# Kernel optimization log

Measured on AMD Instinct MI355X. Metric: run time of the kernel, lower is better.

## Reference

```python
import jax, jax.numpy as jnp
import numpy as np

B, C, K = 256, 4096, 32

def setup_inputs() -> dict:
    key = jax.random.key(0)
    k1, k2, k3 = jax.random.split(key, 3)
    input_data = jax.random.normal(k1, (B, C), dtype=jnp.float32)
    adaptive_margin = jax.random.uniform(k2, (B, C), dtype=jnp.float32)
    # labels in [-1, C); -1 entries are padding (masked out, as in the torch code)
    target = jax.random.randint(k3, (B, K), -1, C, dtype=jnp.int64)
    return {"input_data": input_data, "adaptive_margin": adaptive_margin, "target": target}

def reference(input_data, adaptive_margin, target):
    # input_data, adaptive_margin: [B, C]; target: [B, K] with -1 padding
    Bc, Cc = input_data.shape
    valid = target > -1                                  # [B, K]
    t_idx = jnp.where(valid, target, 0)                  # safe gather index
    m_t = jnp.take_along_axis(adaptive_margin, t_idx, axis=1)  # [B, K]
    x_t = jnp.take_along_axis(input_data, t_idx, axis=1)       # [B, K]
    # pairwise: 1 + (m_t - m_j) - (x_t - x_j) over all classes j, [B, K, C]
    diff = 1.0 + (m_t[:, :, None] - adaptive_margin[:, None, :]) \
               - (x_t[:, :, None] - input_data[:, None, :])
    # exclude j == t and padded labels
    cls = jnp.arange(Cc, dtype=target.dtype)
    keep = valid[:, :, None] & (cls[None, None, :] != t_idx[:, :, None])
    loss = jnp.sum(jnp.where(keep, jax.nn.relu(diff), 0.0))
    return loss / Cc  # size_average=False (default)
```

## Files before the change

### kernel.cpp

```cpp
#include <hip/hip_runtime.h>


#define BB 256
#define CC 4096
#define KK 32
#define THREADS 256

__global__ __launch_bounds__(THREADS) void mlam_rows(
    const float* __restrict__ input,
    const float* __restrict__ margin,
    const int* __restrict__ target,
    float* __restrict__ partials) {

    __shared__ float sc[CC];
    __shared__ float sa[KK];
    __shared__ int   svalid;
    __shared__ float swave[THREADS / 64];

    const int b   = blockIdx.x;
    const int tid = threadIdx.x;
    const float* in_row = input  + (size_t)b * CC;
    const float* mg_row = margin + (size_t)b * CC;

    const float4* in4 = (const float4*)in_row;
    const float4* mg4 = (const float4*)mg_row;
    float4* sc4 = (float4*)sc;
#pragma unroll
    for (int i = 0; i < CC / 4 / THREADS; ++i) {
        int idx = tid + i * THREADS;
        float4 x = in4[idx];
        float4 m = mg4[idx];
        sc4[idx] = make_float4(x.x - m.x, x.y - m.y, x.z - m.z, x.w - m.w);
    }
    if (tid == 0) svalid = 0;
    __syncthreads();

    if (tid < KK) {
        int t = target[b * KK + tid];
        if (t >= 0) {
            sa[tid] = 1.0f + mg_row[t] - in_row[t];
            atomicAdd(&svalid, 1);
        } else {
            sa[tid] = -1e30f;
        }
    }
    __syncthreads();

    float a[KK];
#pragma unroll
    for (int k = 0; k < KK; ++k) a[k] = sa[k];

    float acc = 0.0f;
#pragma unroll
    for (int i = 0; i < CC / 4 / THREADS; ++i) {
        float4 c = sc4[tid + i * THREADS];
#pragma unroll
        for (int k = 0; k < KK; ++k) {
            acc += fmaxf(a[k] + c.x, 0.0f);
            acc += fmaxf(a[k] + c.y, 0.0f);
            acc += fmaxf(a[k] + c.z, 0.0f);
            acc += fmaxf(a[k] + c.w, 0.0f);
        }
    }

#pragma unroll
    for (int off = 32; off > 0; off >>= 1)
        acc += __shfl_down(acc, off, 64);
    if ((tid & 63) == 0) swave[tid >> 6] = acc;
    __syncthreads();
    if (tid == 0) {
        float tot = 0.0f;
#pragma unroll
        for (int w = 0; w < THREADS / 64; ++w) tot += swave[w];
        partials[b] = tot - (float)svalid;
    }
}

__global__ __launch_bounds__(THREADS) void mlam_reduce(
    const float* __restrict__ partials,
    float* __restrict__ out) {
    __shared__ float swave[THREADS / 64];
    const int tid = threadIdx.x;
    float v = partials[tid];
#pragma unroll
    for (int off = 32; off > 0; off >>= 1)
        v += __shfl_down(v, off, 64);
    if ((tid & 63) == 0) swave[tid >> 6] = v;
    __syncthreads();
    if (tid == 0) {
        float tot = 0.0f;
#pragma unroll
        for (int w = 0; w < THREADS / 64; ++w) tot += swave[w];
        out[0] = tot * (1.0f / (float)CC);
    }
}

extern "C" void kernel_launch(void* const* d_in, const int* in_sizes, int n_in,
                              void* d_out, int out_size, void* d_ws, size_t ws_size,
                              hipStream_t stream) {
    const float* input  = (const float*)d_in[0];
    const float* margin = (const float*)d_in[1];
    const int*   target = (const int*)d_in[2];
    float* out      = (float*)d_out;
    float* partials = (float*)d_ws;

    mlam_rows<<<BB, THREADS, 0, stream>>>(input, margin, target, partials);
    mlam_reduce<<<1, THREADS, 0, stream>>>(partials, out);
}
```

Measured before the change: 66.23 us.

## Fuse row and reduce kernels with atomic accumulation and one column per thread

Raises block size to 1024 threads so each thread holds exactly one float4 of the row in registers, which removes the shared-memory staging buffer. The separate reduction kernel is dropped: each block atomically adds its scaled partial into the output, which is zeroed by a memset first. Four independent accumulators break the serial add dependency chain. The memset adds a stream operation, and float atomics make the summation order nondeterministic.

After: 66.47 us. Within noise of the previous version (+0.4%).

```diff
diff --git a/kernel.cpp b/kernel.cpp
--- a/kernel.cpp
+++ b/kernel.cpp
@@ -4,34 +4,28 @@
 #define BB 256
 #define CC 4096
 #define KK 32
-#define THREADS 256
+#define THREADS 1024
+#define NWAVES (THREADS / 64)
 
-__global__ __launch_bounds__(THREADS) void mlam_rows(
+__global__ __launch_bounds__(THREADS) void mlam_fused(
     const float* __restrict__ input,
     const float* __restrict__ margin,
     const int* __restrict__ target,
-    float* __restrict__ partials) {
+    float* __restrict__ out) {
 
-    __shared__ float sc[CC];
     __shared__ float sa[KK];
     __shared__ int   svalid;
-    __shared__ float swave[THREADS / 64];
+    __shared__ float swave[NWAVES];
 
     const int b   = blockIdx.x;
     const int tid = threadIdx.x;
     const float* in_row = input  + (size_t)b * CC;
     const float* mg_row = margin + (size_t)b * CC;
 
-    const float4* in4 = (const float4*)in_row;
-    const float4* mg4 = (const float4*)mg_row;
-    float4* sc4 = (float4*)sc;
-#pragma unroll
-    for (int i = 0; i < CC / 4 / THREADS; ++i) {
-        int idx = tid + i * THREADS;
-        float4 x = in4[idx];
-        float4 m = mg4[idx];
-        sc4[idx] = make_float4(x.x - m.x, x.y - m.y, x.z - m.z, x.w - m.w);
-    }
+    float4 x = ((const float4*)in_row)[tid];
+    float4 m = ((const float4*)mg_row)[tid];
+    float4 c = make_float4(x.x - m.x, x.y - m.y, x.z - m.z, x.w - m.w);
+
     if (tid == 0) svalid = 0;
     __syncthreads();
 
@@ -50,18 +44,16 @@
 #pragma unroll
     for (int k = 0; k < KK; ++k) a[k] = sa[k];
 
-    float acc = 0.0f;
+    float acc0 = 0.f, acc1 = 0.f, acc2 = 0.f, acc3 = 0.f;
 #pragma unroll
-    for (int i = 0; i < CC / 4 / THREADS; ++i) {
-        float4 c = sc4[tid + i * THREADS];
-#pragma unroll
-        for (int k = 0; k < KK; ++k) {
-            acc += fmaxf(a[k] + c.x, 0.0f);
-            acc += fmaxf(a[k] + c.y, 0.0f);
-            acc += fmaxf(a[k] + c.z, 0.0f);
-            acc += fmaxf(a[k] + c.w, 0.0f);
-        }
+    for (int k = 0; k < KK; ++k) {
+        float ak = a[k];
+        acc0 += fmaxf(ak + c.x, 0.0f);
+        acc1 += fmaxf(ak + c.y, 0.0f);
+        acc2 += fmaxf(ak + c.z, 0.0f);
+        acc3 += fmaxf(ak + c.w, 0.0f);
     }
+    float acc = (acc0 + acc1) + (acc2 + acc3);
 
 #pragma unroll
     for (int off = 32; off > 0; off >>= 1)
@@ -71,27 +63,8 @@
     if (tid == 0) {
         float tot = 0.0f;
 #pragma unroll
-        for (int w = 0; w < THREADS / 64; ++w) tot += swave[w];
-        partials[b] = tot - (float)svalid;
-    }
-}
-
-__global__ __launch_bounds__(THREADS) void mlam_reduce(
-    const float* __restrict__ partials,
-    float* __restrict__ out) {
-    __shared__ float swave[THREADS / 64];
-    const int tid = threadIdx.x;
-    float v = partials[tid];
-#pragma unroll
-    for (int off = 32; off > 0; off >>= 1)
-        v += __shfl_down(v, off, 64);
-    if ((tid & 63) == 0) swave[tid >> 6] = v;
-    __syncthreads();
-    if (tid == 0) {
-        float tot = 0.0f;
-#pragma unroll
-        for (int w = 0; w < THREADS / 64; ++w) tot += swave[w];
-        out[0] = tot * (1.0f / (float)CC);
+        for (int w = 0; w < NWAVES; ++w) tot += swave[w];
+        atomicAdd(out, (tot - (float)svalid) * (1.0f / (float)CC));
     }
 }
 
@@ -101,9 +74,8 @@
     const float* input  = (const float*)d_in[0];
     const float* margin = (const float*)d_in[1];
     const int*   target = (const int*)d_in[2];
-    float* out      = (float*)d_out;
-    float* partials = (float*)d_ws;
+    float* out = (float*)d_out;
 
-    mlam_rows<<<BB, THREADS, 0, stream>>>(input, margin, target, partials);
-    mlam_reduce<<<1, THREADS, 0, stream>>>(partials, out);
+    hipMemsetAsync(out, 0, sizeof(float), stream);
+    mlam_fused<<<BB, THREADS, 0, stream>>>(input, margin, target, out);
 }
```
